# Performance work log

Measured on AMD Instinct MI355X. Metric: run time of the kernel, lower is better.

The kernel has to match this reference:

```python
import jax, jax.numpy as jnp
import numpy as np

D, E, H, K = 1024, 8, 4096, 2
B, S = 4, 2048


def setup_inputs() -> dict:
    key = jax.random.key(0)
    ks = jax.random.split(key, 5)
    scale = 0.02
    return {
        "x": jax.random.normal(ks[0], (B, S, D), dtype=jnp.float32),
        "gate_w": jax.random.normal(ks[1], (D, E), dtype=jnp.float32) * scale,
        "w1": jax.random.normal(ks[2], (E, D, H), dtype=jnp.float32) * scale,
        "b1": jnp.zeros((E, H), dtype=jnp.float32),
        "w2": jax.random.normal(ks[3], (E, H, D), dtype=jnp.float32) * scale,
        "b2": jnp.zeros((E, D), dtype=jnp.float32),
        "top_k": K,
    }


def reference(x, gate_w, w1, b1, w2, b2, top_k):
    orig_shape = x.shape
    d = x.shape[-1]
    xt = x.reshape(-1, d)                      # [T, D]
    T = xt.shape[0]

    # Gating: top-k over expert scores, softmax over the selected k.
    scores = xt @ gate_w                       # [T, E]
    expert_weights, expert_indices = jax.lax.top_k(scores, top_k)  # [T, K]
    expert_weights = jax.nn.softmax(expert_weights, axis=-1)

    # Dense all-expert MLP (GPT-style fc -> GELU -> proj), batched over experts.
    h = jnp.einsum('td,edh->eth', xt, w1) + b1[:, None, :]   # [E, T, H]
    h = jax.nn.gelu(h, approximate=False)
    outs = jnp.einsum('eth,ehd->etd', h, w2) + b2[:, None, :]  # [E, T, D]

    # Combine: gather each token's selected experts and mix with gate weights.
    tok = jnp.arange(T)[:, None]               # [T, 1]
    gathered = outs[expert_indices, tok]       # [T, K, D]
    y = jnp.sum(gathered * expert_weights[..., None], axis=1)  # [T, D]
    return y.reshape(orig_shape)
```

## Files before the change

kernel.cpp:

```cpp
#include <hip/hip_runtime.h>
#include <stdint.h>

#define T_TOK 8192
#define D_DIM 1024
#define E_NUM 8
#define H_DIM 4096

#define BM 128
#define BN 128
#define BK 64
#define NSEG 16
#define MAX_ROWS2 18432
#define MAX_MT2 (MAX_ROWS2/BM)

typedef unsigned short u16;
typedef __attribute__((ext_vector_type(8))) short shortx8;
typedef __attribute__((ext_vector_type(4))) float floatx4;
typedef __attribute__((ext_vector_type(8))) unsigned short ushortx8;

typedef const __attribute__((address_space(1))) unsigned int g_uint;
typedef __attribute__((address_space(3))) unsigned int l_uint;

__device__ __forceinline__ u16 f2bf(float f) {
  union { float f; unsigned int u; } v; v.f = f;
  unsigned int r = v.u + 0x7FFFu + ((v.u >> 16) & 1u);
  return (u16)(r >> 16);
}
__device__ __forceinline__ float bf2f(u16 u) {
  union { unsigned int u; float f; } v; v.u = ((unsigned int)u) << 16; return v.f;
}
__device__ __forceinline__ void gld_lds16(const u16* g, u16* l) {
  __builtin_amdgcn_global_load_lds((g_uint*)g, (l_uint*)l, 16, 0, 0);
}

__global__ __launch_bounds__(256) void init_kernel(int* counts, int* fills, int* row_token) {
  int i = blockIdx.x * 256 + threadIdx.x;
  if (i < MAX_ROWS2) row_token[i] = -1;
  if (blockIdx.x == 0 && threadIdx.x < NSEG) { counts[threadIdx.x] = 0; fills[threadIdx.x] = 0; }
}

__global__ __launch_bounds__(256) void convert_x_kernel(const float* __restrict__ X, u16* __restrict__ XC) {
  size_t i = ((size_t)blockIdx.x * 256 + threadIdx.x) * 8;
  float4 a = *(const float4*)&X[i];
  float4 b = *(const float4*)&X[i + 4];
  ushortx8 o;
  o[0] = f2bf(a.x); o[1] = f2bf(a.y); o[2] = f2bf(a.z); o[3] = f2bf(a.w);
  o[4] = f2bf(b.x); o[5] = f2bf(b.y); o[6] = f2bf(b.z); o[7] = f2bf(b.w);
  *(ushortx8*)&XC[i] = o;
}

__global__ __launch_bounds__(256) void gate_kernel(const float* __restrict__ X, const float* __restrict__ GW,
                                                   int* __restrict__ tk_idx, float* __restrict__ tk_w,
                                                   int* __restrict__ counts) {
  const int lane = threadIdx.x & 63;
  const int t = blockIdx.x * 4 + (threadIdx.x >> 6);
  const float* xr = X + (size_t)t * D_DIM + lane * 16;
  float acc[E_NUM];
#pragma unroll
  for (int e = 0; e < E_NUM; e++) acc[e] = 0.f;
#pragma unroll
  for (int i = 0; i < 16; i++) {
    float xv = xr[i];
    const float* g = GW + (size_t)(lane * 16 + i) * E_NUM;
#pragma unroll
    for (int e = 0; e < E_NUM; e++) acc[e] += xv * g[e];
  }
#pragma unroll
  for (int e = 0; e < E_NUM; e++)
    for (int off = 32; off; off >>= 1) acc[e] += __shfl_xor(acc[e], off);
  if (lane == 0) {
    int i0 = 0; float v0 = acc[0];
#pragma unroll
    for (int e = 1; e < E_NUM; e++) if (acc[e] > v0) { v0 = acc[e]; i0 = e; }
    int i1 = -1; float v1 = -1e30f;
#pragma unroll
    for (int e = 0; e < E_NUM; e++) if (e != i0 && acc[e] > v1) { v1 = acc[e]; i1 = e; }
    float e1 = expf(v1 - v0);
    float inv = 1.f / (1.f + e1);
    tk_idx[t * 2] = i0; tk_idx[t * 2 + 1] = i1;
    tk_w[t * 2] = inv;  tk_w[t * 2 + 1] = e1 * inv;
    atomicAdd(&counts[i0], 1); atomicAdd(&counts[E_NUM + i1], 1);
  }
}

__global__ void prefix_kernel(const int* counts, int* seg) {
  if (threadIdx.x == 0 && blockIdx.x == 0) {
    int a = 0;
    for (int i = 0; i < NSEG; i++) { seg[i] = a; a += ((counts[i] + BM - 1) / BM) * BM; }
    seg[NSEG] = a;
  }
}

__global__ __launch_bounds__(256) void fill_kernel(const int* __restrict__ tk_idx, const float* __restrict__ tk_w,
                                                   const int* __restrict__ seg, int* __restrict__ fills,
                                                   int* __restrict__ row_token, float* __restrict__ row_weight) {
  int t = blockIdx.x * 256 + threadIdx.x;
  if (t >= T_TOK) return;
#pragma unroll
  for (int s = 0; s < 2; s++) {
    int sidx = s * E_NUM + tk_idx[t * 2 + s];
    int pos = atomicAdd(&fills[sidx], 1);
    int r = seg[sidx] + pos;
    row_token[r] = t; row_weight[r] = tk_w[t * 2 + s];
  }
}

__global__ __launch_bounds__(256) void transpose_kernel(const float* __restrict__ src, u16* __restrict__ dst,
                                                        int R, int C) {
  __shared__ u16 tile[32][33];
  int tx = threadIdx.x & 31, ty = threadIdx.x >> 5;
  size_t off = (size_t)blockIdx.z * R * C;
  int r0 = blockIdx.y * 32, c0 = blockIdx.x * 32;
#pragma unroll
  for (int i = 0; i < 32; i += 8) tile[ty + i][tx] = f2bf(src[off + (size_t)(r0 + ty + i) * C + c0 + tx]);
  __syncthreads();
#pragma unroll
  for (int i = 0; i < 32; i += 8) dst[off + (size_t)(c0 + ty + i) * R + r0 + tx] = tile[tx][ty + i];
}

__global__ __launch_bounds__(256, 2) void fc1_kernel(const u16* __restrict__ XC, const u16* __restrict__ W1T,
                                                     const float* __restrict__ B1, u16* __restrict__ Hbuf,
                                                     const int* __restrict__ row_token, const int* __restrict__ seg,
                                                     int mtile0, int e_filter) {
  const int mtile = mtile0 + blockIdx.y, ntile = blockIdx.x;
  const int row0 = mtile * BM;
  if (row0 >= seg[NSEG]) return;
  int sidx = 0;
#pragma unroll
  for (int i = 1; i < NSEG; i++) if (row0 >= seg[i]) sidx = i;
  const int e = sidx & 7;
  if (e_filter >= 0 && e != e_filter) return;
  const size_t ebase = (e_filter >= 0) ? 0 : (size_t)e * H_DIM;
  const u16* Bbase = W1T + (ebase + (size_t)ntile * BN) * D_DIM;

  __shared__ u16 lA[BM * BK];
  __shared__ u16 lB[BN * BK];
  const int tid = threadIdx.x;
  const u16* gA[4]; const u16* gB[4];
#pragma unroll
  for (int r = 0; r < 4; r++) {
    int c = r * 256 + tid;
    int arow = c >> 3, acol = (c & 7) * 8;
    int tok = row_token[row0 + arow]; if (tok < 0) tok = 0;
    gA[r] = XC + (size_t)tok * D_DIM + acol;
    gB[r] = Bbase + (size_t)arow * D_DIM + acol;
  }
  const int lane = tid & 63;
  const int mq = (tid >> 7) & 1, nq = (tid >> 6) & 1;
  const int lrow = lane & 15, quad = lane >> 4;
  floatx4 acc[4][4];
#pragma unroll
  for (int i = 0; i < 4; i++)
#pragma unroll
    for (int j = 0; j < 4; j++)
#pragma unroll
      for (int r = 0; r < 4; r++) acc[i][j][r] = 0.f;

  for (int k0 = 0; k0 < D_DIM; k0 += BK) {
#pragma unroll
    for (int r = 0; r < 4; r++) gld_lds16(gA[r] + k0, &lA[(r * 256 + tid) * 8]);
#pragma unroll
    for (int r = 0; r < 4; r++) gld_lds16(gB[r] + k0, &lB[(r * 256 + tid) * 8]);
    __syncthreads();
#pragma unroll
    for (int kk = 0; kk < 2; kk++) {
      shortx8 af[4], bfr[4];
#pragma unroll
      for (int i = 0; i < 4; i++) af[i]  = *(const shortx8*)&lA[(mq * 64 + i * 16 + lrow) * BK + kk * 32 + quad * 8];
#pragma unroll
      for (int i = 0; i < 4; i++) bfr[i] = *(const shortx8*)&lB[(nq * 64 + i * 16 + lrow) * BK + kk * 32 + quad * 8];
#pragma unroll
      for (int i = 0; i < 4; i++)
#pragma unroll
        for (int j = 0; j < 4; j++)
          acc[i][j] = __builtin_amdgcn_mfma_f32_16x16x32_bf16(af[i], bfr[j], acc[i][j], 0, 0, 0);
    }
    __syncthreads();
  }
#pragma unroll
  for (int j = 0; j < 4; j++) {
    float bv = B1[(size_t)e * H_DIM + ntile * BN + nq * 64 + j * 16 + lrow];
#pragma unroll
    for (int i = 0; i < 4; i++)
#pragma unroll
      for (int rr = 0; rr < 4; rr++) {
        int hrow = (mtile - mtile0) * BM + mq * 64 + i * 16 + quad * 4 + rr;
        float v = acc[i][j][rr] + bv;
        float gv = 0.5f * v * (1.f + erff(v * 0.70710678118654752f));
        Hbuf[(size_t)hrow * H_DIM + (size_t)ntile * BN + nq * 64 + j * 16 + lrow] = f2bf(gv);
      }
  }
}

__global__ __launch_bounds__(256, 2) void fc2_kernel(const u16* __restrict__ Hbuf, const u16* __restrict__ W2T,
                                                     const float* __restrict__ B2, float* __restrict__ out,
                                                     const int* __restrict__ row_token, const float* __restrict__ row_weight,
                                                     const int* __restrict__ seg,
                                                     int mtile0, int e_filter, int slot_filter) {
  const int mtile = mtile0 + blockIdx.y, ntile = blockIdx.x;
  const int row0 = mtile * BM;
  if (row0 >= seg[NSEG]) return;
  int sidx = 0;
#pragma unroll
  for (int i = 1; i < NSEG; i++) if (row0 >= seg[i]) sidx = i;
  const int e = sidx & 7, slot = sidx >> 3;
  if (slot != slot_filter) return;
  if (e_filter >= 0 && e != e_filter) return;
  const size_t ebase = (e_filter >= 0) ? 0 : (size_t)e * D_DIM;
  const u16* Bbase = W2T + (ebase + (size_t)ntile * BN) * H_DIM;

  __shared__ u16 lA[BM * BK];
  __shared__ u16 lB[BN * BK];
  const int tid = threadIdx.x;
  const u16* gA[4]; const u16* gB[4];
#pragma unroll
  for (int r = 0; r < 4; r++) {
    int c = r * 256 + tid;
    int arow = c >> 3, acol = (c & 7) * 8;
    gA[r] = Hbuf + (size_t)((mtile - mtile0) * BM + arow) * H_DIM + acol;
    gB[r] = Bbase + (size_t)arow * H_DIM + acol;
  }
  const int lane = tid & 63;
  const int mq = (tid >> 7) & 1, nq = (tid >> 6) & 1;
  const int lrow = lane & 15, quad = lane >> 4;
  floatx4 acc[4][4];
#pragma unroll
  for (int i = 0; i < 4; i++)
#pragma unroll
    for (int j = 0; j < 4; j++)
#pragma unroll
      for (int r = 0; r < 4; r++) acc[i][j][r] = 0.f;

  for (int k0 = 0; k0 < H_DIM; k0 += BK) {
#pragma unroll
    for (int r = 0; r < 4; r++) gld_lds16(gA[r] + k0, &lA[(r * 256 + tid) * 8]);
#pragma unroll
    for (int r = 0; r < 4; r++) gld_lds16(gB[r] + k0, &lB[(r * 256 + tid) * 8]);
    __syncthreads();
#pragma unroll
    for (int kk = 0; kk < 2; kk++) {
      shortx8 af[4], bfr[4];
#pragma unroll
      for (int i = 0; i < 4; i++) af[i]  = *(const shortx8*)&lA[(mq * 64 + i * 16 + lrow) * BK + kk * 32 + quad * 8];
#pragma unroll
      for (int i = 0; i < 4; i++) bfr[i] = *(const shortx8*)&lB[(nq * 64 + i * 16 + lrow) * BK + kk * 32 + quad * 8];
#pragma unroll
      for (int i = 0; i < 4; i++)
#pragma unroll
        for (int j = 0; j < 4; j++)
          acc[i][j] = __builtin_amdgcn_mfma_f32_16x16x32_bf16(af[i], bfr[j], acc[i][j], 0, 0, 0);
    }
    __syncthreads();
  }
#pragma unroll
  for (int i = 0; i < 4; i++)
#pragma unroll
    for (int rr = 0; rr < 4; rr++) {
      int gr = row0 + mq * 64 + i * 16 + quad * 4 + rr;
      int tok = row_token[gr];
      if (tok >= 0) {
        float wgt = row_weight[gr];
        size_t base = (size_t)tok * D_DIM + (size_t)ntile * BN + nq * 64 + lrow;
#pragma unroll
        for (int j = 0; j < 4; j++) {
          float bv = B2[(size_t)e * D_DIM + ntile * BN + nq * 64 + j * 16 + lrow];
          float val = (acc[i][j][rr] + bv) * wgt;
          if (slot_filter == 0) out[base + j * 16] = val;
          else                  out[base + j * 16] += val;
        }
      }
    }
}

__global__ __launch_bounds__(256) void zero_out_kernel(float* out) {
  size_t i = (size_t)blockIdx.x * 256 + threadIdx.x;
  out[i] = 0.f;
}

extern "C" void kernel_launch(void* const* d_in, const int* in_sizes, int n_in,
                              void* d_out, int out_size, void* d_ws, size_t ws_size,
                              hipStream_t stream) {
  const float* x  = (const float*)d_in[0];
  const float* gw = (const float*)d_in[1];
  const float* w1 = (const float*)d_in[2];
  const float* b1 = (const float*)d_in[3];
  const float* w2 = (const float*)d_in[4];
  const float* b2 = (const float*)d_in[5];
  float* out = (float*)d_out;

  char* p = (char*)d_ws;
  auto alloc = [&](size_t n) { char* q = p; p += (n + 255) & ~(size_t)255; return q; };
  int*   counts     = (int*)alloc(NSEG * 4);
  int*   fills      = (int*)alloc(NSEG * 4);
  int*   seg        = (int*)alloc((NSEG + 1) * 4);
  int*   tk_idx     = (int*)alloc((size_t)T_TOK * 2 * 4);
  float* tk_w       = (float*)alloc((size_t)T_TOK * 2 * 4);
  int*   row_token  = (int*)alloc((size_t)MAX_ROWS2 * 4);
  float* row_weight = (float*)alloc((size_t)MAX_ROWS2 * 4);
  u16*   xc         = (u16*)alloc((size_t)T_TOK * D_DIM * 2);
  size_t meta = (size_t)(p - (char*)d_ws);

  const size_t W64b = (size_t)E_NUM * H_DIM * D_DIM * 2;
  const size_t W8b  = (size_t)H_DIM * D_DIM * 2;
  auto hbytes = [](int n) { int cm = (MAX_MT2 + n - 1) / n; return (size_t)cm * BM * H_DIM * 2; };

  int mode = 2, N = 1;
  {
    const int cand[6] = {1, 2, 4, 8, 16, 32};
    for (int ci = 0; ci < 6 && mode == 2; ci++)
      if (meta + W64b + hbytes(cand[ci]) <= ws_size) { mode = 0; N = cand[ci]; }
    for (int ci = 0; ci < 6 && mode == 2; ci++)
      if (meta + W8b + hbytes(cand[ci]) <= ws_size) { mode = 1; N = cand[ci]; }
  }

  if (mode == 2) {
    zero_out_kernel<<<(int)(((size_t)T_TOK * D_DIM) / 256), 256, 0, stream>>>(out);
    return;
  }

  u16* W    = (u16*)alloc(mode == 0 ? W64b : W8b);
  u16* Hbuf = (u16*)alloc(hbytes(N));
  const int cm = (MAX_MT2 + N - 1) / N;

  init_kernel<<<(MAX_ROWS2 + 255) / 256, 256, 0, stream>>>(counts, fills, row_token);
  convert_x_kernel<<<(int)(((size_t)T_TOK * D_DIM) / 2048), 256, 0, stream>>>(x, xc);
  gate_kernel<<<T_TOK / 4, 256, 0, stream>>>(x, gw, tk_idx, tk_w, counts);
  prefix_kernel<<<1, 64, 0, stream>>>(counts, seg);
  fill_kernel<<<T_TOK / 256, 256, 0, stream>>>(tk_idx, tk_w, seg, fills, row_token, row_weight);

  for (int c = 0; c < N; ++c) {
    int mtile0 = c * cm;
    int cmc = MAX_MT2 - mtile0; if (cmc > cm) cmc = cm; if (cmc <= 0) break;
    if (mode == 0) {
      transpose_kernel<<<dim3(H_DIM / 32, D_DIM / 32, E_NUM), 256, 0, stream>>>(w1, W, D_DIM, H_DIM);
      fc1_kernel<<<dim3(H_DIM / BN, cmc), 256, 0, stream>>>(xc, W, b1, Hbuf, row_token, seg, mtile0, -1);
      transpose_kernel<<<dim3(D_DIM / 32, H_DIM / 32, E_NUM), 256, 0, stream>>>(w2, W, H_DIM, D_DIM);
      fc2_kernel<<<dim3(D_DIM / BN, cmc), 256, 0, stream>>>(Hbuf, W, b2, out, row_token, row_weight, seg, mtile0, -1, 0);
      fc2_kernel<<<dim3(D_DIM / BN, cmc), 256, 0, stream>>>(Hbuf, W, b2, out, row_token, row_weight, seg, mtile0, -1, 1);
    } else {
      for (int e = 0; e < E_NUM; e++) {
        transpose_kernel<<<dim3(H_DIM / 32, D_DIM / 32, 1), 256, 0, stream>>>(w1 + (size_t)e * D_DIM * H_DIM, W, D_DIM, H_DIM);
        fc1_kernel<<<dim3(H_DIM / BN, cmc), 256, 0, stream>>>(xc, W, b1, Hbuf, row_token, seg, mtile0, e);
      }
      for (int s = 0; s < 2; s++)
        for (int e = 0; e < E_NUM; e++) {
          transpose_kernel<<<dim3(D_DIM / 32, H_DIM / 32, 1), 256, 0, stream>>>(w2 + (size_t)e * H_DIM * D_DIM, W, H_DIM, D_DIM);
          fc2_kernel<<<dim3(D_DIM / BN, cmc), 256, 0, stream>>>(Hbuf, W, b2, out, row_token, row_weight, seg, mtile0, e, s);
        }
    }
  }
}
```

Baseline: 1.109 ms.

## Merge routing slots per expert, split-K fc2 with atomics, fast GELU, hoisted transposes

Routing segments are now per expert (8 instead of 16), so each token's two slots share one expert segment and padding shrinks. fc2 gains a split-K grid dimension and accumulates into a pre-zeroed output with atomic adds, replacing the two ordered slot passes. Other changes: a tanh-style sigmoid GELU approximation replaces erff, occupancy hints rise to 3, the gate loads are vectorised, and weight transposes are hoisted out of the chunk loop when the workspace fits both. The GELU approximation and atomic float accumulation change numerics and make summation order nondeterministic.

```diff
diff --git a/kernel.cpp b/kernel.cpp
--- a/kernel.cpp
+++ b/kernel.cpp
@@ -9,9 +9,10 @@
 #define BM 128
 #define BN 128
 #define BK 64
-#define NSEG 16
-#define MAX_ROWS2 18432
+#define NSEG 8
+#define MAX_ROWS2 17408
 #define MAX_MT2 (MAX_ROWS2/BM)
+#define KSPLIT 2
 
 typedef unsigned short u16;
 typedef __attribute__((ext_vector_type(8))) short shortx8;
@@ -26,17 +27,24 @@
   unsigned int r = v.u + 0x7FFFu + ((v.u >> 16) & 1u);
   return (u16)(r >> 16);
 }
-__device__ __forceinline__ float bf2f(u16 u) {
-  union { unsigned int u; float f; } v; v.u = ((unsigned int)u) << 16; return v.f;
-}
 __device__ __forceinline__ void gld_lds16(const u16* g, u16* l) {
   __builtin_amdgcn_global_load_lds((g_uint*)g, (l_uint*)l, 16, 0, 0);
+}
+__device__ __forceinline__ float gelu_fast(float v) {
+  float y = v * (1.5957691216f + 0.07135481627f * v * v);
+  y = fminf(y, 30.f);
+  float ey = __expf(y);
+  return v * ey * __builtin_amdgcn_rcpf(1.f + ey);
 }
 
 __global__ __launch_bounds__(256) void init_kernel(int* counts, int* fills, int* row_token) {
   int i = blockIdx.x * 256 + threadIdx.x;
   if (i < MAX_ROWS2) row_token[i] = -1;
   if (blockIdx.x == 0 && threadIdx.x < NSEG) { counts[threadIdx.x] = 0; fills[threadIdx.x] = 0; }
+}
+
+__global__ __launch_bounds__(256) void zero4_kernel(float4* out) {
+  out[(size_t)blockIdx.x * 256 + threadIdx.x] = float4{0.f, 0.f, 0.f, 0.f};
 }
 
 __global__ __launch_bounds__(256) void convert_x_kernel(const float* __restrict__ X, u16* __restrict__ XC) {
@@ -54,16 +62,22 @@
                                                    int* __restrict__ counts) {
   const int lane = threadIdx.x & 63;
   const int t = blockIdx.x * 4 + (threadIdx.x >> 6);
-  const float* xr = X + (size_t)t * D_DIM + lane * 16;
+  const float4* xr4 = (const float4*)(X + (size_t)t * D_DIM + lane * 16);
+  const float4* gw4 = (const float4*)GW;
   float acc[E_NUM];
 #pragma unroll
   for (int e = 0; e < E_NUM; e++) acc[e] = 0.f;
 #pragma unroll
-  for (int i = 0; i < 16; i++) {
-    float xv = xr[i];
-    const float* g = GW + (size_t)(lane * 16 + i) * E_NUM;
-#pragma unroll
-    for (int e = 0; e < E_NUM; e++) acc[e] += xv * g[e];
+  for (int i4 = 0; i4 < 4; i4++) {
+    float4 xv = xr4[i4];
+#pragma unroll
+    for (int c = 0; c < 4; c++) {
+      float xs = (&xv.x)[c];
+      int d = lane * 16 + i4 * 4 + c;
+      float4 g0 = gw4[d * 2], g1 = gw4[d * 2 + 1];
+      acc[0] += xs * g0.x; acc[1] += xs * g0.y; acc[2] += xs * g0.z; acc[3] += xs * g0.w;
+      acc[4] += xs * g1.x; acc[5] += xs * g1.y; acc[6] += xs * g1.z; acc[7] += xs * g1.w;
+    }
   }
 #pragma unroll
   for (int e = 0; e < E_NUM; e++)
@@ -79,7 +93,7 @@
     float inv = 1.f / (1.f + e1);
     tk_idx[t * 2] = i0; tk_idx[t * 2 + 1] = i1;
     tk_w[t * 2] = inv;  tk_w[t * 2 + 1] = e1 * inv;
-    atomicAdd(&counts[i0], 1); atomicAdd(&counts[E_NUM + i1], 1);
+    atomicAdd(&counts[i0], 1); atomicAdd(&counts[i1], 1);
   }
 }
 
@@ -98,7 +112,7 @@
   if (t >= T_TOK) return;
 #pragma unroll
   for (int s = 0; s < 2; s++) {
-    int sidx = s * E_NUM + tk_idx[t * 2 + s];
+    int sidx = tk_idx[t * 2 + s];
     int pos = atomicAdd(&fills[sidx], 1);
     int r = seg[sidx] + pos;
     row_token[r] = t; row_weight[r] = tk_w[t * 2 + s];
@@ -118,7 +132,7 @@
   for (int i = 0; i < 32; i += 8) dst[off + (size_t)(c0 + ty + i) * R + r0 + tx] = tile[tx][ty + i];
 }
 
-__global__ __launch_bounds__(256, 2) void fc1_kernel(const u16* __restrict__ XC, const u16* __restrict__ W1T,
+__global__ __launch_bounds__(256, 3) void fc1_kernel(const u16* __restrict__ XC, const u16* __restrict__ W1T,
                                                      const float* __restrict__ B1, u16* __restrict__ Hbuf,
                                                      const int* __restrict__ row_token, const int* __restrict__ seg,
                                                      int mtile0, int e_filter) {
@@ -128,7 +142,7 @@
   int sidx = 0;
 #pragma unroll
   for (int i = 1; i < NSEG; i++) if (row0 >= seg[i]) sidx = i;
-  const int e = sidx & 7;
+  const int e = sidx;
   if (e_filter >= 0 && e != e_filter) return;
   const size_t ebase = (e_filter >= 0) ? 0 : (size_t)e * H_DIM;
   const u16* Bbase = W1T + (ebase + (size_t)ntile * BN) * D_DIM;
@@ -186,25 +200,24 @@
       for (int rr = 0; rr < 4; rr++) {
         int hrow = (mtile - mtile0) * BM + mq * 64 + i * 16 + quad * 4 + rr;
         float v = acc[i][j][rr] + bv;
-        float gv = 0.5f * v * (1.f + erff(v * 0.70710678118654752f));
-        Hbuf[(size_t)hrow * H_DIM + (size_t)ntile * BN + nq * 64 + j * 16 + lrow] = f2bf(gv);
+        Hbuf[(size_t)hrow * H_DIM + (size_t)ntile * BN + nq * 64 + j * 16 + lrow] = f2bf(gelu_fast(v));
       }
   }
 }
 
-__global__ __launch_bounds__(256, 2) void fc2_kernel(const u16* __restrict__ Hbuf, const u16* __restrict__ W2T,
+__global__ __launch_bounds__(256, 3) void fc2_kernel(const u16* __restrict__ Hbuf, const u16* __restrict__ W2T,
                                                      const float* __restrict__ B2, float* __restrict__ out,
                                                      const int* __restrict__ row_token, const float* __restrict__ row_weight,
                                                      const int* __restrict__ seg,
-                                                     int mtile0, int e_filter, int slot_filter) {
+                                                     int mtile0, int e_filter) {
   const int mtile = mtile0 + blockIdx.y, ntile = blockIdx.x;
+  const int kz = blockIdx.z;
   const int row0 = mtile * BM;
   if (row0 >= seg[NSEG]) return;
   int sidx = 0;
 #pragma unroll
   for (int i = 1; i < NSEG; i++) if (row0 >= seg[i]) sidx = i;
-  const int e = sidx & 7, slot = sidx >> 3;
-  if (slot != slot_filter) return;
+  const int e = sidx;
   if (e_filter >= 0 && e != e_filter) return;
   const size_t ebase = (e_filter >= 0) ? 0 : (size_t)e * D_DIM;
   const u16* Bbase = W2T + (ebase + (size_t)ntile * BN) * H_DIM;
@@ -231,7 +244,9 @@
 #pragma unroll
       for (int r = 0; r < 4; r++) acc[i][j][r] = 0.f;
 
-  for (int k0 = 0; k0 < H_DIM; k0 += BK) {
+  const int kbeg = kz * (H_DIM / KSPLIT);
+  const int kend = kbeg + (H_DIM / KSPLIT);
+  for (int k0 = kbeg; k0 < kend; k0 += BK) {
 #pragma unroll
     for (int r = 0; r < 4; r++) gld_lds16(gA[r] + k0, &lA[(r * 256 + tid) * 8]);
 #pragma unroll
@@ -263,18 +278,12 @@
         size_t base = (size_t)tok * D_DIM + (size_t)ntile * BN + nq * 64 + lrow;
 #pragma unroll
         for (int j = 0; j < 4; j++) {
-          float bv = B2[(size_t)e * D_DIM + ntile * BN + nq * 64 + j * 16 + lrow];
+          float bv = (kz == 0) ? B2[(size_t)e * D_DIM + ntile * BN + nq * 64 + j * 16 + lrow] : 0.f;
           float val = (acc[i][j][rr] + bv) * wgt;
-          if (slot_filter == 0) out[base + j * 16] = val;
-          else                  out[base + j * 16] += val;
+          unsafeAtomicAdd(&out[base + j * 16], val);
         }
       }
     }
-}
-
-__global__ __launch_bounds__(256) void zero_out_kernel(float* out) {
-  size_t i = (size_t)blockIdx.x * 256 + threadIdx.x;
-  out[i] = 0.f;
 }
 
 extern "C" void kernel_launch(void* const* d_in, const int* in_sizes, int n_in,
@@ -300,25 +309,29 @@
   u16*   xc         = (u16*)alloc((size_t)T_TOK * D_DIM * 2);
   size_t meta = (size_t)(p - (char*)d_ws);
 
-  const size_t W64b = (size_t)E_NUM * H_DIM * D_DIM * 2;
-  const size_t W8b  = (size_t)H_DIM * D_DIM * 2;
-  auto hbytes = [](int n) { int cm = (MAX_MT2 + n - 1) / n; return (size_t)cm * BM * H_DIM * 2; };
-
-  int mode = 2, N = 1;
+  const size_t Wfull = (size_t)E_NUM * H_DIM * D_DIM * 2;
+  const size_t Wone  = (size_t)H_DIM * D_DIM * 2;
+  auto hbytes = [](int n) { int cmx = (MAX_MT2 + n - 1) / n; return (size_t)cmx * BM * H_DIM * 2; };
+
+  int mode = 3, N = 1;
   {
     const int cand[6] = {1, 2, 4, 8, 16, 32};
-    for (int ci = 0; ci < 6 && mode == 2; ci++)
-      if (meta + W64b + hbytes(cand[ci]) <= ws_size) { mode = 0; N = cand[ci]; }
-    for (int ci = 0; ci < 6 && mode == 2; ci++)
-      if (meta + W8b + hbytes(cand[ci]) <= ws_size) { mode = 1; N = cand[ci]; }
-  }
-
-  if (mode == 2) {
-    zero_out_kernel<<<(int)(((size_t)T_TOK * D_DIM) / 256), 256, 0, stream>>>(out);
+    for (int ci = 0; ci < 6 && mode == 3; ci++)
+      if (meta + 2 * Wfull + hbytes(cand[ci]) <= ws_size) { mode = 0; N = cand[ci]; }
+    for (int ci = 0; ci < 6 && mode == 3; ci++)
+      if (meta + Wfull + hbytes(cand[ci]) <= ws_size) { mode = 1; N = cand[ci]; }
+    for (int ci = 0; ci < 6 && mode == 3; ci++)
+      if (meta + Wone + hbytes(cand[ci]) <= ws_size) { mode = 2; N = cand[ci]; }
+  }
+
+  if (mode == 3) {
+    zero4_kernel<<<(int)(((size_t)T_TOK * D_DIM) / 1024), 256, 0, stream>>>((float4*)out);
     return;
   }
 
-  u16* W    = (u16*)alloc(mode == 0 ? W64b : W8b);
+  u16 *W1T, *W2T;
+  if (mode == 0) { W1T = (u16*)alloc(Wfull); W2T = (u16*)alloc(Wfull); }
+  else           { W1T = W2T = (u16*)alloc(mode == 1 ? Wfull : Wone); }
   u16* Hbuf = (u16*)alloc(hbytes(N));
   const int cm = (MAX_MT2 + N - 1) / N;
 
@@ -327,26 +340,33 @@
   gate_kernel<<<T_TOK / 4, 256, 0, stream>>>(x, gw, tk_idx, tk_w, counts);
   prefix_kernel<<<1, 64, 0, stream>>>(counts, seg);
   fill_kernel<<<T_TOK / 256, 256, 0, stream>>>(tk_idx, tk_w, seg, fills, row_token, row_weight);
+  zero4_kernel<<<(int)(((size_t)T_TOK * D_DIM) / 1024), 256, 0, stream>>>((float4*)out);
+
+  if (mode == 0) {
+    transpose_kernel<<<dim3(H_DIM / 32, D_DIM / 32, E_NUM), 256, 0, stream>>>(w1, W1T, D_DIM, H_DIM);
+    transpose_kernel<<<dim3(D_DIM / 32, H_DIM / 32, E_NUM), 256, 0, stream>>>(w2, W2T, H_DIM, D_DIM);
+  }
 
   for (int c = 0; c < N; ++c) {
     int mtile0 = c * cm;
     int cmc = MAX_MT2 - mtile0; if (cmc > cm) cmc = cm; if (cmc <= 0) break;
     if (mode == 0) {
-      transpose_kernel<<<dim3(H_DIM / 32, D_DIM / 32, E_NUM), 256, 0, stream>>>(w1, W, D_DIM, H_DIM);
-      fc1_kernel<<<dim3(H_DIM / BN, cmc), 256, 0, stream>>>(xc, W, b1, Hbuf, row_token, seg, mtile0, -1);
-      transpose_kernel<<<dim3(D_DIM / 32, H_DIM / 32, E_NUM), 256, 0, stream>>>(w2, W, H_DIM, D_DIM);
-      fc2_kernel<<<dim3(D_DIM / BN, cmc), 256, 0, stream>>>(Hbuf, W, b2, out, row_token, row_weight, seg, mtile0, -1, 0);
-      fc2_kernel<<<dim3(D_DIM / BN, cmc), 256, 0, stream>>>(Hbuf, W, b2, out, row_token, row_weight, seg, mtile0, -1, 1);
+      fc1_kernel<<<dim3(H_DIM / BN, cmc), 256, 0, stream>>>(xc, W1T, b1, Hbuf, row_token, seg, mtile0, -1);
+      fc2_kernel<<<dim3(D_DIM / BN, cmc, KSPLIT), 256, 0, stream>>>(Hbuf, W2T, b2, out, row_token, row_weight, seg, mtile0, -1);
+    } else if (mode == 1) {
+      transpose_kernel<<<dim3(H_DIM / 32, D_DIM / 32, E_NUM), 256, 0, stream>>>(w1, W1T, D_DIM, H_DIM);
+      fc1_kernel<<<dim3(H_DIM / BN, cmc), 256, 0, stream>>>(xc, W1T, b1, Hbuf, row_token, seg, mtile0, -1);
+      transpose_kernel<<<dim3(D_DIM / 32, H_DIM / 32, E_NUM), 256, 0, stream>>>(w2, W2T, H_DIM, D_DIM);
+      fc2_kernel<<<dim3(D_DIM / BN, cmc, KSPLIT), 256, 0, stream>>>(Hbuf, W2T, b2, out, row_token, row_weight, seg, mtile0, -1);
     } else {
       for (int e = 0; e < E_NUM; e++) {
-        transpose_kernel<<<dim3(H_DIM / 32, D_DIM / 32, 1), 256, 0, stream>>>(w1 + (size_t)e * D_DIM * H_DIM, W, D_DIM, H_DIM);
-        fc1_kernel<<<dim3(H_DIM / BN, cmc), 256, 0, stream>>>(xc, W, b1, Hbuf, row_token, seg, mtile0, e);
+        transpose_kernel<<<dim3(H_DIM / 32, D_DIM / 32, 1), 256, 0, stream>>>(w1 + (size_t)e * D_DIM * H_DIM, W1T, D_DIM, H_DIM);
+        fc1_kernel<<<dim3(H_DIM / BN, cmc), 256, 0, stream>>>(xc, W1T, b1, Hbuf, row_token, seg, mtile0, e);
       }
-      for (int s = 0; s < 2; s++)
-        for (int e = 0; e < E_NUM; e++) {
-          transpose_kernel<<<dim3(D_DIM / 32, H_DIM / 32, 1), 256, 0, stream>>>(w2 + (size_t)e * H_DIM * D_DIM, W, H_DIM, D_DIM);
-          fc2_kernel<<<dim3(D_DIM / BN, cmc), 256, 0, stream>>>(Hbuf, W, b2, out, row_token, row_weight, seg, mtile0, e, s);
-        }
-    }
-  }
-}
+      for (int e = 0; e < E_NUM; e++) {
+        transpose_kernel<<<dim3(D_DIM / 32, H_DIM / 32, 1), 256, 0, stream>>>(w2 + (size_t)e * H_DIM * D_DIM, W2T, H_DIM, D_DIM);
+        fc2_kernel<<<dim3(D_DIM / BN, cmc, KSPLIT), 256, 0, stream>>>(Hbuf, W2T, b2, out, row_token, row_weight, seg, mtile0, e);
+      }
+    }
+  }
+}
```

Measured after the change: 1.085 ms. -2.2%, faster.
